# Performance work log

Hardware: AMD Instinct MI355X
Metric: run time of the kernel (lower is better)

Reference implementation:

```python
import jax, jax.numpy as jnp
import numpy as np

N_NODES = 50000
N_EDGES = 500000
V_IN, V_OUT, E_IN, E_OUT = 128, 128, 64, 64
SQRT_TWO = 1.4142135623730951

def _xavier_normal(key, shape, gain):
    fan_in, fan_out = shape
    std = gain * np.sqrt(2.0 / (fan_in + fan_out))
    return jax.random.normal(key, shape, dtype=jnp.float32) * std

def setup_inputs() -> dict:
    key = jax.random.key(0)
    ks = jax.random.split(key, 8)
    cat_dim = 2 * V_IN + E_IN
    return {
        "x": jax.random.normal(ks[0], (N_NODES, V_IN), dtype=jnp.float32),
        "edge_index": jax.random.randint(ks[1], (2, N_EDGES), 0, N_NODES, dtype=jnp.int64),
        "edge_attr": jax.random.normal(ks[2], (N_EDGES, E_IN), dtype=jnp.float32),
        "W_a": _xavier_normal(ks[3], (cat_dim, V_OUT), SQRT_TWO),
        "W_T": _xavier_normal(ks[4], (cat_dim, V_OUT), SQRT_TWO),
        "b_T": jnp.zeros((V_OUT,), dtype=jnp.float32),
        "W_e": _xavier_normal(ks[5], (V_IN, E_OUT), SQRT_TWO),
        "W_ee": _xavier_normal(ks[6], (E_IN, E_OUT), SQRT_TWO),
        "a_prelu": jnp.array(0.25, dtype=jnp.float32),  # PReLU default: single shared slope
    }

def _prelu(x, a):
    return jnp.where(x >= 0, x, a * x)

def _scatter_softmax(src, index, num_segments):
    # src: [E, D], index: [E] -> softmax over edges grouped by index, per column
    seg_max = jax.ops.segment_max(src, index, num_segments=num_segments)  # [N, D]
    ex = jnp.exp(src - seg_max[index])
    seg_sum = jax.ops.segment_sum(ex, index, num_segments=num_segments)  # [N, D]
    return ex / (seg_sum[index] + 1e-16)

def reference(x, edge_index, edge_attr, W_a, W_T, b_T, W_e, W_ee, a_prelu):
    src, dst = edge_index[0], edge_index[1]
    N1 = x[src]          # [E, V_IN]
    N2 = x[dst]          # [E, V_IN]
    e = edge_attr        # [E, E_IN]
    new_e_feat = N1 @ W_e + N2 @ W_e + e @ W_ee          # [E, E_OUT]
    cat = jnp.concatenate([N2, e, N1], axis=1)            # [E, 2V+E]
    attention_logits = _prelu(cat @ W_a, a_prelu)         # [E, V_OUT]
    messages = cat @ W_T                                  # [E, V_OUT]
    attention = _scatter_softmax(attention_logits, dst, x.shape[0])
    agg_msg = attention * messages
    new_x = jax.ops.segment_sum(agg_msg, dst, num_segments=x.shape[0]) + b_T
    return (new_x, new_e_feat)
```

## Files before the change

kernel.cpp:

```cpp
#include <hip/hip_runtime.h>
#include <hip/hip_bf16.h>


typedef float  f32x4   __attribute__((ext_vector_type(4)));
typedef __bf16 bf16x8  __attribute__((ext_vector_type(8)));
typedef unsigned short ushort8_t __attribute__((ext_vector_type(8)));

#define ROWSTRIDE 328
#define RED_STRIDE 132

__device__ __forceinline__ unsigned short f2bf(float f) {
  unsigned int u = __float_as_uint(f);
  return (unsigned short)((u + 0x7FFFu + ((u >> 16) & 1u)) >> 16);
}

__device__ __forceinline__ void store_bf4(unsigned short* p, float4 v) {
  ushort4 u;
  u.x = f2bf(v.x); u.y = f2bf(v.y); u.z = f2bf(v.z); u.w = f2bf(v.w);
  *(ushort4*)p = u;
}

__global__ void prep_b_kernel(const float* __restrict__ Wa,
                              const float* __restrict__ Wt,
                              const float* __restrict__ We,
                              const float* __restrict__ Wee,
                              unsigned short* __restrict__ Bp) {
  int pe = blockIdx.x * 256 + threadIdx.x;
  int j    = pe & 7;
  int lane = (pe >> 3) & 63;
  int kt   = (pe >> 9) % 10;
  int nt   = pe / 5120;
  int k = kt * 32 + ((lane >> 4) << 3) + j;
  int n = nt * 16 + (lane & 15);
  float v;
  if (n < 128) {
    v = Wa[k * 128 + n];
  } else if (n < 256) {
    v = Wt[k * 128 + (n - 128)];
  } else {
    int c = n - 256;
    if (k < 128)      v = We[k * 64 + c];
    else if (k < 192) v = Wee[(k - 128) * 64 + c];
    else              v = We[(k - 192) * 64 + c];
  }
  Bp[pe] = f2bf(v);
}

__global__ void hist_kernel(const int* __restrict__ ei, int* __restrict__ cnt,
                            int E) {
  int e = blockIdx.x * 256 + threadIdx.x;
  if (e < E) atomicAdd(&cnt[ei[E + e]], 1);
}

__global__ void scan_kernel(const int* __restrict__ cnt, int* __restrict__ cur,
                            int n) {
  __shared__ int ls[1024];
  const int t = threadIdx.x;
  const int base = t * 49;
  int s = 0;
  for (int i = 0; i < 49; ++i) {
    int idx = base + i;
    if (idx < n) s += cnt[idx];
  }
  ls[t] = s;
  __syncthreads();
  for (int off = 1; off < 1024; off <<= 1) {
    int v = (t >= off) ? ls[t - off] : 0;
    __syncthreads();
    ls[t] += v;
    __syncthreads();
  }
  int run = (t == 0) ? 0 : ls[t - 1];
  for (int i = 0; i < 49; ++i) {
    int idx = base + i;
    if (idx < n) {
      int v = cnt[idx];
      cur[idx] = run;
      run += v;
    }
  }
}

__global__ void scatter_kernel(const int* __restrict__ ei, int* __restrict__ cur,
                               int* __restrict__ perm, int E) {
  int e = blockIdx.x * 256 + threadIdx.x;
  if (e < E) {
    int d = ei[E + e];
    int pos = atomicAdd(&cur[d], 1);
    perm[pos] = e;
  }
}

__global__ __launch_bounds__(256, 2) void fused_edge_kernel(
    const float* __restrict__ x,
    const int*   __restrict__ ei,
    const float* __restrict__ ea,
    const int*   __restrict__ perm,
    const unsigned short* __restrict__ Bp,
    float* __restrict__ num,
    float* __restrict__ den,
    float* __restrict__ out_e,
    const float* __restrict__ a_prelu,
    int E) {
  __shared__ __align__(16) char smem[64 * ROWSTRIDE * 2];
  unsigned short* At = (unsigned short*)smem;
  float* red = (float*)smem;
  __shared__ int s_src[64];
  __shared__ int s_dst[64];
  __shared__ int s_eid[64];

  const int tid = threadIdx.x;
  const int eb  = blockIdx.x * 64;
  const int nvalid = min(64, E - eb);

  if (tid < 64) {
    int e = 0, s = 0, d = 0;
    if (tid < nvalid) {
      e = perm[eb + tid];
      s = ei[e];
      d = ei[E + e];
    }
    s_eid[tid] = e;
    s_src[tid] = s;
    s_dst[tid] = d;
  }
  __syncthreads();

  const float4* x4  = (const float4*)x;
  const float4* ea4 = (const float4*)ea;

  #pragma unroll
  for (int i = tid; i < 2048; i += 256) {
    int r = i >> 5, c4 = i & 31;
    float4 v = {0.f, 0.f, 0.f, 0.f};
    if (r < nvalid) v = x4[(size_t)s_dst[r] * 32 + c4];
    store_bf4(&At[r * ROWSTRIDE + c4 * 4], v);
  }
  #pragma unroll
  for (int i = tid; i < 1024; i += 256) {
    int r = i >> 4, c4 = i & 15;
    float4 v = {0.f, 0.f, 0.f, 0.f};
    if (r < nvalid) v = ea4[(size_t)s_eid[r] * 16 + c4];
    store_bf4(&At[r * ROWSTRIDE + 128 + c4 * 4], v);
  }
  #pragma unroll
  for (int i = tid; i < 2048; i += 256) {
    int r = i >> 5, c4 = i & 31;
    float4 v = {0.f, 0.f, 0.f, 0.f};
    if (r < nvalid) v = x4[(size_t)s_src[r] * 32 + c4];
    store_bf4(&At[r * ROWSTRIDE + 192 + c4 * 4], v);
  }
  __syncthreads();

  const int w    = tid >> 6;
  const int l    = tid & 63;
  const int lrow = l & 15;
  const int lk8  = (l >> 4) << 3;

  f32x4 acc[4][5];
  #pragma unroll
  for (int mt = 0; mt < 4; ++mt)
    #pragma unroll
    for (int i = 0; i < 5; ++i)
      acc[mt][i] = (f32x4){0.f, 0.f, 0.f, 0.f};

  for (int kc = 0; kc < 10; ++kc) {
    const int kbase = kc * 32 + lk8;
    bf16x8 av[4];
    #pragma unroll
    for (int mt = 0; mt < 4; ++mt) {
      ushort8_t u = *(const ushort8_t*)&At[(mt * 16 + lrow) * ROWSTRIDE + kbase];
      av[mt] = __builtin_bit_cast(bf16x8, u);
    }
    #pragma unroll
    for (int i = 0; i < 5; ++i) {
      const int nt = w + 4 * i;
      ushort8_t ub = *(const ushort8_t*)&Bp[(((nt * 10 + kc) * 64) + l) * 8];
      bf16x8 bv = __builtin_bit_cast(bf16x8, ub);
      #pragma unroll
      for (int mt = 0; mt < 4; ++mt)
        acc[mt][i] = __builtin_amdgcn_mfma_f32_16x16x32_bf16(av[mt], bv, acc[mt][i], 0, 0, 0);
    }
  }

  const float slope = a_prelu[0];
  const int rbase = (l >> 4) << 2;
  const int ccol  = l & 15;

  #pragma unroll
  for (int mt = 0; mt < 4; ++mt) {
    const int m0 = mt * 16 + rbase;
    #pragma unroll
    for (int r = 0; r < 4; ++r) {
      int m = m0 + r;
      if (m < nvalid)
        out_e[(size_t)s_eid[m] * 64 + w * 16 + ccol] = acc[mt][4][r];
    }
  }

  float exv[4][2][4];
  #pragma unroll
  for (int mt = 0; mt < 4; ++mt)
    #pragma unroll
    for (int i2 = 0; i2 < 2; ++i2)
      #pragma unroll
      for (int r = 0; r < 4; ++r) {
        float lg = acc[mt][i2][r];
        exv[mt][i2][r] = __expf(lg >= 0.f ? lg : slope * lg);
      }

  __syncthreads();

  #pragma unroll
  for (int mt = 0; mt < 4; ++mt) {
    const int m0 = mt * 16 + rbase;
    #pragma unroll
    for (int i2 = 0; i2 < 2; ++i2) {
      const int c = (w + 4 * i2) * 16 + ccol;
      #pragma unroll
      for (int r = 0; r < 4; ++r)
        red[(m0 + r) * RED_STRIDE + c] = exv[mt][i2][r] * acc[mt][i2 + 2][r];
    }
  }
  __syncthreads();
  {
    const int c  = tid & 127;
    const int r0 = (tid >> 7) * 32;
    const int r1 = min(r0 + 32, nvalid);
    float sum = 0.f;
    for (int r = r0; r < r1; ++r) {
      sum += red[r * RED_STRIDE + c];
      if (r == r1 - 1 || s_dst[r + 1] != s_dst[r]) {
        unsafeAtomicAdd(&num[(size_t)s_dst[r] * 128 + c], sum);
        sum = 0.f;
      }
    }
  }
  __syncthreads();

  #pragma unroll
  for (int mt = 0; mt < 4; ++mt) {
    const int m0 = mt * 16 + rbase;
    #pragma unroll
    for (int i2 = 0; i2 < 2; ++i2) {
      const int c = (w + 4 * i2) * 16 + ccol;
      #pragma unroll
      for (int r = 0; r < 4; ++r)
        red[(m0 + r) * RED_STRIDE + c] = exv[mt][i2][r];
    }
  }
  __syncthreads();
  {
    const int c  = tid & 127;
    const int r0 = (tid >> 7) * 32;
    const int r1 = min(r0 + 32, nvalid);
    float sum = 0.f;
    for (int r = r0; r < r1; ++r) {
      sum += red[r * RED_STRIDE + c];
      if (r == r1 - 1 || s_dst[r + 1] != s_dst[r]) {
        unsafeAtomicAdd(&den[(size_t)s_dst[r] * 128 + c], sum);
        sum = 0.f;
      }
    }
  }
}

__global__ void finalize_kernel(const float* __restrict__ num,
                                const float* __restrict__ den,
                                const float* __restrict__ bT,
                                float* __restrict__ out_x,
                                int total) {
  int i = blockIdx.x * 256 + threadIdx.x;
  if (i < total)
    out_x[i] = num[i] / (den[i] + 1e-16f) + bT[i & 127];
}

extern "C" void kernel_launch(void* const* d_in, const int* in_sizes, int n_in,
                              void* d_out, int out_size, void* d_ws, size_t ws_size,
                              hipStream_t stream) {
  const float* x   = (const float*)d_in[0];
  const int*   ei  = (const int*)d_in[1];
  const float* ea  = (const float*)d_in[2];
  const float* Wa  = (const float*)d_in[3];
  const float* Wt  = (const float*)d_in[4];
  const float* bT  = (const float*)d_in[5];
  const float* We  = (const float*)d_in[6];
  const float* Wee = (const float*)d_in[7];
  const float* ap  = (const float*)d_in[8];

  const int N = in_sizes[0] / 128;
  const int E = in_sizes[1] / 2;

  char* ws = (char*)d_ws;
  unsigned short* Bp = (unsigned short*)ws;
  float* num = (float*)(ws + 204800);
  float* den = num + (size_t)N * 128;
  int* cnt   = (int*)(ws + 204800 + (size_t)N * 128 * 8);
  int* cur   = cnt + 50176;
  int* perm  = cur + 50176;

  float* out_x = (float*)d_out;
  float* out_e = out_x + (size_t)N * 128;

  hipMemsetAsync(num, 0, (size_t)N * 128 * 8 + 50176 * sizeof(int), stream);
  prep_b_kernel<<<400, 256, 0, stream>>>(Wa, Wt, We, Wee, Bp);
  hist_kernel<<<(E + 255) / 256, 256, 0, stream>>>(ei, cnt, E);
  scan_kernel<<<1, 1024, 0, stream>>>(cnt, cur, N);
  scatter_kernel<<<(E + 255) / 256, 256, 0, stream>>>(ei, cur, perm, E);
  fused_edge_kernel<<<(E + 63) / 64, 256, 0, stream>>>(x, ei, ea, perm, Bp,
                                                       num, den, out_e, ap, E);
  finalize_kernel<<<((size_t)N * 128 + 255) / 256, 256, 0, stream>>>(
      num, den, bT, out_x, N * 128);
}
```

Before: 692.7 us.

## Precast x to bf16, parallelize CSR scan, and pre-sort src/dst indices

Adds a pass that converts x to bf16 once, so the edge kernel gathers half as many bytes per node row and skips per-edge conversion. Replaces the single-block serial scan with a three-kernel multi-block scan. The scatter step now writes sorted src and dst arrays alongside edge ids, which removes the dependent indirect loads of edge_index in the edge kernel. In exchange it adds extra kernel launches and workspace traffic for the bf16 copy and the sorted index arrays.

Measured after the change: 585.8 us. 15.4% less time.

```diff
diff --git a/kernel.cpp b/kernel.cpp
--- a/kernel.cpp
+++ b/kernel.cpp
@@ -46,56 +46,88 @@
   Bp[pe] = f2bf(v);
 }
 
+__global__ void xbf16_kernel(const float* __restrict__ x,
+                             unsigned short* __restrict__ xb, int total4) {
+  int i = blockIdx.x * 256 + threadIdx.x;
+  if (i < total4) {
+    float4 v = ((const float4*)x)[i];
+    store_bf4(&xb[(size_t)i * 4], v);
+  }
+}
+
 __global__ void hist_kernel(const int* __restrict__ ei, int* __restrict__ cnt,
                             int E) {
   int e = blockIdx.x * 256 + threadIdx.x;
   if (e < E) atomicAdd(&cnt[ei[E + e]], 1);
 }
 
-__global__ void scan_kernel(const int* __restrict__ cnt, int* __restrict__ cur,
-                            int n) {
-  __shared__ int ls[1024];
-  const int t = threadIdx.x;
-  const int base = t * 49;
-  int s = 0;
-  for (int i = 0; i < 49; ++i) {
-    int idx = base + i;
-    if (idx < n) s += cnt[idx];
-  }
-  ls[t] = s;
-  __syncthreads();
-  for (int off = 1; off < 1024; off <<= 1) {
-    int v = (t >= off) ? ls[t - off] : 0;
-    __syncthreads();
-    ls[t] += v;
-    __syncthreads();
-  }
-  int run = (t == 0) ? 0 : ls[t - 1];
-  for (int i = 0; i < 49; ++i) {
-    int idx = base + i;
-    if (idx < n) {
-      int v = cnt[idx];
-      cur[idx] = run;
-      run += v;
-    }
-  }
+__global__ void scan1_kernel(const int* __restrict__ cnt,
+                             int* __restrict__ bsum, int n) {
+  __shared__ int ls[256];
+  int t = threadIdx.x;
+  int i = blockIdx.x * 256 + t;
+  ls[t] = (i < n) ? cnt[i] : 0;
+  __syncthreads();
+  for (int off = 128; off > 0; off >>= 1) {
+    if (t < off) ls[t] += ls[t + off];
+    __syncthreads();
+  }
+  if (t == 0) bsum[blockIdx.x] = ls[0];
+}
+
+__global__ void scan2_kernel(int* __restrict__ bsum, int nb) {
+  __shared__ int ls[256];
+  int t = threadIdx.x;
+  int v = (t < nb) ? bsum[t] : 0;
+  ls[t] = v;
+  __syncthreads();
+  for (int off = 1; off < 256; off <<= 1) {
+    int u = (t >= off) ? ls[t - off] : 0;
+    __syncthreads();
+    ls[t] += u;
+    __syncthreads();
+  }
+  if (t < nb) bsum[t] = ls[t] - v;
+}
+
+__global__ void scan3_kernel(const int* __restrict__ cnt,
+                             const int* __restrict__ bsum,
+                             int* __restrict__ cur, int n) {
+  __shared__ int ls[256];
+  int t = threadIdx.x;
+  int i = blockIdx.x * 256 + t;
+  int v = (i < n) ? cnt[i] : 0;
+  ls[t] = v;
+  __syncthreads();
+  for (int off = 1; off < 256; off <<= 1) {
+    int u = (t >= off) ? ls[t - off] : 0;
+    __syncthreads();
+    ls[t] += u;
+    __syncthreads();
+  }
+  if (i < n) cur[i] = ls[t] - v + bsum[blockIdx.x];
 }
 
 __global__ void scatter_kernel(const int* __restrict__ ei, int* __restrict__ cur,
-                               int* __restrict__ perm, int E) {
+                               int* __restrict__ eid_s, int* __restrict__ src_s,
+                               int* __restrict__ dst_s, int E) {
   int e = blockIdx.x * 256 + threadIdx.x;
   if (e < E) {
+    int s = ei[e];
     int d = ei[E + e];
     int pos = atomicAdd(&cur[d], 1);
-    perm[pos] = e;
+    eid_s[pos] = e;
+    src_s[pos] = s;
+    dst_s[pos] = d;
   }
 }
 
 __global__ __launch_bounds__(256, 2) void fused_edge_kernel(
-    const float* __restrict__ x,
-    const int*   __restrict__ ei,
+    const unsigned short* __restrict__ xb,
     const float* __restrict__ ea,
-    const int*   __restrict__ perm,
+    const int*   __restrict__ eid_s,
+    const int*   __restrict__ src_s,
+    const int*   __restrict__ dst_s,
     const unsigned short* __restrict__ Bp,
     float* __restrict__ num,
     float* __restrict__ den,
@@ -116,9 +148,9 @@
   if (tid < 64) {
     int e = 0, s = 0, d = 0;
     if (tid < nvalid) {
-      e = perm[eb + tid];
-      s = ei[e];
-      d = ei[E + e];
+      e = eid_s[eb + tid];
+      s = src_s[eb + tid];
+      d = dst_s[eb + tid];
     }
     s_eid[tid] = e;
     s_src[tid] = s;
@@ -126,15 +158,15 @@
   }
   __syncthreads();
 
-  const float4* x4  = (const float4*)x;
-  const float4* ea4 = (const float4*)ea;
-
-  #pragma unroll
-  for (int i = tid; i < 2048; i += 256) {
-    int r = i >> 5, c4 = i & 31;
-    float4 v = {0.f, 0.f, 0.f, 0.f};
-    if (r < nvalid) v = x4[(size_t)s_dst[r] * 32 + c4];
-    store_bf4(&At[r * ROWSTRIDE + c4 * 4], v);
+  const ushort8_t* xb8 = (const ushort8_t*)xb;
+  const float4*    ea4 = (const float4*)ea;
+
+  #pragma unroll
+  for (int i = tid; i < 1024; i += 256) {
+    int r = i >> 4, c = i & 15;
+    ushort8_t v = {0, 0, 0, 0, 0, 0, 0, 0};
+    if (r < nvalid) v = xb8[(size_t)s_dst[r] * 16 + c];
+    *(ushort8_t*)&At[r * ROWSTRIDE + c * 8] = v;
   }
   #pragma unroll
   for (int i = tid; i < 1024; i += 256) {
@@ -144,11 +176,11 @@
     store_bf4(&At[r * ROWSTRIDE + 128 + c4 * 4], v);
   }
   #pragma unroll
-  for (int i = tid; i < 2048; i += 256) {
-    int r = i >> 5, c4 = i & 31;
-    float4 v = {0.f, 0.f, 0.f, 0.f};
-    if (r < nvalid) v = x4[(size_t)s_src[r] * 32 + c4];
-    store_bf4(&At[r * ROWSTRIDE + 192 + c4 * 4], v);
+  for (int i = tid; i < 1024; i += 256) {
+    int r = i >> 4, c = i & 15;
+    ushort8_t v = {0, 0, 0, 0, 0, 0, 0, 0};
+    if (r < nvalid) v = xb8[(size_t)s_src[r] * 16 + c];
+    *(ushort8_t*)&At[r * ROWSTRIDE + 192 + c * 8] = v;
   }
   __syncthreads();
 
@@ -290,6 +322,7 @@
 
   const int N = in_sizes[0] / 128;
   const int E = in_sizes[1] / 2;
+  const int NB = (N + 255) / 256;
 
   char* ws = (char*)d_ws;
   unsigned short* Bp = (unsigned short*)ws;
@@ -297,18 +330,26 @@
   float* den = num + (size_t)N * 128;
   int* cnt   = (int*)(ws + 204800 + (size_t)N * 128 * 8);
   int* cur   = cnt + 50176;
-  int* perm  = cur + 50176;
+  int* eid_s = cur + 50176;
+  int* src_s = eid_s + 500224;
+  int* dst_s = src_s + 500224;
+  int* bsum  = dst_s + 500224;
+  unsigned short* x_bf16 = (unsigned short*)(bsum + 256);
 
   float* out_x = (float*)d_out;
   float* out_e = out_x + (size_t)N * 128;
 
   hipMemsetAsync(num, 0, (size_t)N * 128 * 8 + 50176 * sizeof(int), stream);
   prep_b_kernel<<<400, 256, 0, stream>>>(Wa, Wt, We, Wee, Bp);
+  xbf16_kernel<<<(N * 32 + 255) / 256, 256, 0, stream>>>(x, x_bf16, N * 32);
   hist_kernel<<<(E + 255) / 256, 256, 0, stream>>>(ei, cnt, E);
-  scan_kernel<<<1, 1024, 0, stream>>>(cnt, cur, N);
-  scatter_kernel<<<(E + 255) / 256, 256, 0, stream>>>(ei, cur, perm, E);
-  fused_edge_kernel<<<(E + 63) / 64, 256, 0, stream>>>(x, ei, ea, perm, Bp,
-                                                       num, den, out_e, ap, E);
+  scan1_kernel<<<NB, 256, 0, stream>>>(cnt, bsum, N);
+  scan2_kernel<<<1, 256, 0, stream>>>(bsum, NB);
+  scan3_kernel<<<NB, 256, 0, stream>>>(cnt, bsum, cur, N);
+  scatter_kernel<<<(E + 255) / 256, 256, 0, stream>>>(ei, cur, eid_s, src_s,
+                                                      dst_s, E);
+  fused_edge_kernel<<<(E + 63) / 64, 256, 0, stream>>>(
+      x_bf16, ea, eid_s, src_s, dst_s, Bp, num, den, out_e, ap, E);
   finalize_kernel<<<((size_t)N * 128 + 255) / 256, 256, 0, stream>>>(
       num, den, bT, out_x, N * 128);
 }
```
